# Kernel tuning notes

Measured on AMD Instinct MI355X. Metric: run time of the kernel, lower is better.

The kernel has to match this reference:

```python
import jax, jax.numpy as jnp
import numpy as np
from jax import lax

C = 128; NH = 8; DH = 16      # attn_channels, heads, head_dim
DI = 256; DS = 16; DC = 4     # hmb d_inner=expand*C, d_state, d_conv
KTOP = 128                    # max(min_focus_tokens, int(W*0.5))
CR = 64; CI = 128             # radar / image channels


def _ln(x, g, b, eps=1e-5):
    m = jnp.mean(x, -1, keepdims=True)
    v = jnp.mean((x - m) ** 2, -1, keepdims=True)
    return (x - m) * lax.rsqrt(v + eps) * g + b


def _conv1x1(x, w):
    return jnp.einsum('bchw,oc->bohw', x, w)


def _forward(image_features, radar_features, W_img, W_rad, g_q, b_q, g_kv, b_kv, g2, b2,
             Ws1, bs1, Ws2, bs2, Wqkv, bqkv, Wo, bo, Wf1, bf1, Wf2, bf2, W_delta,
             gamma, gamma_hmb, Wg, bg, Wfuse, bn_g, bn_b, bn_m, bn_v,
             W_hin, conv_dw, b_dw, W_dt, b_dt, W_Bp, W_Cp, A_log, Dp, W_hout):
    B, Cr, H, W = radar_features.shape
    N = B * H
    img_attn = _conv1x1(image_features, W_img)          # [B,C,H,W]
    rad_attn = _conv1x1(radar_features, W_rad)
    img_seq = img_attn.transpose(0, 2, 3, 1).reshape(N, W, C)
    rad_seq = rad_attn.transpose(0, 2, 3, 1).reshape(N, W, C)
    # progressive focus: per-row top-K image tokens
    si = jnp.concatenate([lax.stop_gradient(rad_seq), img_seq], -1)
    h1 = jax.nn.relu(si @ Ws1.T + bs1)
    score = (h1 @ Ws2.T + bs2)[..., 0]                  # [N,W]
    _, idx = lax.top_k(score, KTOP)
    img_kv = jnp.take_along_axis(img_seq, idx[:, :, None], axis=1)  # [N,K,C]
    # cross attention (torch MultiheadAttention, batch_first)
    q = _ln(rad_seq, g_q, b_q)
    kv = _ln(img_kv, g_kv, b_kv)
    Wq, Wk, Wv = Wqkv[:C], Wqkv[C:2 * C], Wqkv[2 * C:]
    bq_, bk_, bv_ = bqkv[:C], bqkv[C:2 * C], bqkv[2 * C:]
    qh = (q @ Wq.T + bq_).reshape(N, W, NH, DH)
    kh = (kv @ Wk.T + bk_).reshape(N, KTOP, NH, DH)
    vh = (kv @ Wv.T + bv_).reshape(N, KTOP, NH, DH)
    att = jax.nn.softmax(jnp.einsum('nqhd,nkhd->nhqk', qh, kh) / (DH ** 0.5), -1)
    ao = jnp.einsum('nhqk,nkhd->nqhd', att, vh).reshape(N, W, C) @ Wo.T + bo
    rad_seq = rad_seq + ao
    rad_seq = rad_seq + (jax.nn.relu(_ln(rad_seq, g2, b2) @ Wf1.T + bf1) @ Wf2.T + bf2)
    rad_bev = rad_seq.reshape(B, H, W, C).transpose(0, 3, 1, 2)
    delta_attn = _conv1x1(rad_bev, W_delta)
    # HMB-lite: bidirectional selective scan along x (per row)
    xz = _conv1x1(jnp.concatenate([rad_bev, img_attn], 1), W_hin)  # [B,2*DI,H,W]
    x, z = xz[:, :DI], xz[:, DI:]
    xr = x.transpose(0, 2, 1, 3).reshape(N, DI, W)
    zr = z.transpose(0, 2, 3, 1).reshape(N, W, DI)
    xp = jnp.pad(xr, ((0, 0), (0, 0), (DC - 1, 0)))     # causal depthwise conv
    xc = lax.conv_general_dilated(xp, conv_dw[:, None, :], (1,), 'VALID',
                                  feature_group_count=DI,
                                  dimension_numbers=('NCH', 'OIH', 'NCH'))
    xs = jax.nn.silu(xc + b_dw[:, None]).transpose(0, 2, 1)        # [N,W,DI]
    dt = jax.nn.softplus(xs @ W_dt.T + b_dt)            # [N,W,DI]
    Bt = xs @ W_Bp.T                                    # [N,W,DS]
    Ct = xs @ W_Cp.T
    A = -jnp.exp(A_log)                                 # [DI,DS]

    def scan(reverse):
        def step(h, inp):
            x_t, dt_t, B_t, C_t = inp
            h = jnp.exp(dt_t[..., None] * A) * h + (dt_t * x_t)[..., None] * B_t[:, None, :]
            return h, jnp.sum(h * C_t[:, None, :], -1)
        h0 = jnp.zeros((N, DI, DS), xs.dtype)
        seq = (xs.transpose(1, 0, 2), dt.transpose(1, 0, 2),
               Bt.transpose(1, 0, 2), Ct.transpose(1, 0, 2))
        _, ys = lax.scan(step, h0, seq, reverse=reverse)
        return ys.transpose(1, 0, 2)

    y = scan(False) + scan(True) + Dp * xs
    y = y * jax.nn.silu(zr)
    hmb = (y @ W_hout.T).reshape(B, H, W, C).transpose(0, 3, 1, 2)
    delta_hmb = _conv1x1(hmb, W_delta)
    # gate + range mask
    gate = jax.nn.sigmoid(_conv1x1(jnp.concatenate([radar_features, image_features], 1), Wg)
                          + bg[None, :, None, None])
    yv = jnp.arange(H, dtype=radar_features.dtype)
    wmask = jnp.clip(1.0 - 0.7 * yv / (H - 1), 0.3, None)
    gate = gate * wmask[None, None, :, None]
    radar_enh = radar_features + gamma * gate * delta_attn + gamma_hmb * gate * delta_hmb
    fuse_in = jnp.concatenate([radar_enh, image_features], 1)
    fo = lax.conv_general_dilated(fuse_in, Wfuse, (1, 1), 'SAME',
                                  dimension_numbers=('NCHW', 'OIHW', 'NCHW'))
    fo = ((fo - bn_m[None, :, None, None]) * lax.rsqrt(bn_v + 1e-5)[None, :, None, None]
          * bn_g[None, :, None, None] + bn_b[None, :, None, None])
    return jax.nn.relu(fo)


def setup_inputs():
    key = jax.random.key(0)
    ks = list(jax.random.split(key, 24))
    def rn(i, shape, s=0.05):
        return jax.random.normal(ks[i], shape, dtype=jnp.float32) * s
    B, H, W = 2, 256, 256
    return dict(
        image_features=jax.random.normal(ks[0], (B, CI, H, W), jnp.float32),
        radar_features=jax.random.normal(ks[1], (B, CR, H, W), jnp.float32),
        W_img=rn(2, (C, CI)), W_rad=rn(3, (C, CR)),
        g_q=jnp.ones(C), b_q=jnp.zeros(C), g_kv=jnp.ones(C), b_kv=jnp.zeros(C),
        g2=jnp.ones(C), b2=jnp.zeros(C),
        Ws1=rn(4, (64, 2 * C)), bs1=jnp.zeros(64), Ws2=rn(5, (1, 64)), bs2=jnp.zeros(1),
        Wqkv=rn(6, (3 * C, C)), bqkv=jnp.zeros(3 * C), Wo=rn(7, (C, C)), bo=jnp.zeros(C),
        Wf1=rn(8, (4 * C, C)), bf1=jnp.zeros(4 * C), Wf2=rn(9, (C, 4 * C)), bf2=jnp.zeros(C),
        W_delta=rn(10, (CR, C)),
        gamma=jnp.array(0.1, jnp.float32), gamma_hmb=jnp.array(0.05, jnp.float32),
        Wg=rn(11, (CR, CR + CI)), bg=jnp.zeros(CR),
        Wfuse=rn(12, (CR + CI, CR + CI, 3, 3)),
        bn_g=jnp.ones(CR + CI), bn_b=jnp.zeros(CR + CI),
        bn_m=jnp.zeros(CR + CI), bn_v=jnp.ones(CR + CI),
        W_hin=rn(13, (2 * DI, 2 * C)), conv_dw=rn(14, (DI, DC)), b_dw=jnp.zeros(DI),
        W_dt=rn(15, (DI, DI)), b_dt=jnp.full((DI,), 0.5, jnp.float32),
        W_Bp=rn(16, (DS, DI)), W_Cp=rn(17, (DS, DI)),
        A_log=jnp.log(jnp.broadcast_to(jnp.arange(1, DS + 1, dtype=jnp.float32), (DI, DS))),
        Dp=jnp.full((DI,), 0.01, jnp.float32),
        W_hout=rn(18, (C, DI)),
    )


def reference(image_features, radar_features, W_img, W_rad, g_q, b_q, g_kv, b_kv, g2, b2,
              Ws1, bs1, Ws2, bs2, Wqkv, bqkv, Wo, bo, Wf1, bf1, Wf2, bf2, W_delta,
              gamma, gamma_hmb, Wg, bg, Wfuse, bn_g, bn_b, bn_m, bn_v,
              W_hin, conv_dw, b_dw, W_dt, b_dt, W_Bp, W_Cp, A_log, Dp, W_hout):
    return _forward(image_features, radar_features, W_img, W_rad, g_q, b_q, g_kv, b_kv, g2, b2,
                    Ws1, bs1, Ws2, bs2, Wqkv, bqkv, Wo, bo, Wf1, bf1, Wf2, bf2, W_delta,
                    gamma, gamma_hmb, Wg, bg, Wfuse, bn_g, bn_b, bn_m, bn_v,
                    W_hin, conv_dw, b_dw, W_dt, b_dt, W_Bp, W_Cp, A_log, Dp, W_hout)
```

## Files before the change

### kernel.cpp

```cpp
#include <hip/hip_runtime.h>
#include <hip/hip_bf16.h>
#include <cstddef>


#define PTOK   131072
#define WSEQ   256
#define HWPIX  65536

typedef unsigned short u16;
typedef unsigned int   u32;
typedef __bf16 bf16x8 __attribute__((ext_vector_type(8)));
typedef float  f32x4  __attribute__((ext_vector_type(4)));

__device__ __forceinline__ float b2f(u16 u) { return __uint_as_float((u32)u << 16); }
__device__ __forceinline__ u16   f2b(float f) {
    u32 x = __float_as_uint(f);
    return (u16)((x + 0x7fffu + ((x >> 16) & 1u)) >> 16);
}
__device__ __forceinline__ u16 f2b_fast(float f) {
    return __builtin_bit_cast(u16, (__bf16)f);
}
__device__ __forceinline__ u32 pk2(float a, float b) {
    return (u32)f2b(a) | ((u32)f2b(b) << 16);
}
__device__ __forceinline__ void unpack8(uint4 p, float* v) {
    const u32 a[4] = {p.x, p.y, p.z, p.w};
#pragma unroll
    for (int q = 0; q < 4; ++q) {
        v[2 * q]     = b2f((u16)(a[q] & 0xffffu));
        v[2 * q + 1] = b2f((u16)(a[q] >> 16));
    }
}
__device__ __forceinline__ void load32(const u16* p, float* v) {
    uint4 a = *(const uint4*)p, b = *(const uint4*)(p + 8);
    uint4 c = *(const uint4*)(p + 16), d = *(const uint4*)(p + 24);
    unpack8(a, v); unpack8(b, v + 8); unpack8(c, v + 16); unpack8(d, v + 24);
}

constexpr int AM_NCHW = 0, AM_TOK = 1, AM_LN = 2, AM_LNG = 3, AM_CAT = 4, AM_FIN = 5;
constexpr int EP_NONE = 0, EP_RELU = 1, EP_RES = 2, EP_SP = 3;

template<int AM, int EPI>
__global__ __launch_bounds__(256)
void mgemm(const void* __restrict__ Apv, const void* __restrict__ Ap2v,
           const void* __restrict__ Ap3v, const void* __restrict__ Ap4v,
           const int* __restrict__ gidx, const float* __restrict__ stats,
           const float* __restrict__ lng, const float* __restrict__ lnb,
           const float* __restrict__ dpv,
           int K, int Cin,
           const float* __restrict__ Bw, const float* __restrict__ Bw2,
           const float* __restrict__ bias,
           u16* __restrict__ Cout, int O, int Ostride)
{
    __shared__ u16 Als[128 * 72];
    __shared__ u16 Bls[128 * 72];
    const int tid = threadIdx.x;
    const int t0 = blockIdx.x * 128;
    const int o0 = blockIdx.y * 128;
    const int lane = tid & 63, wv = tid >> 6;
    const int wm = (wv & 1) * 64, wn = (wv >> 1) * 64;
    const int fc = lane & 15, quad = lane >> 4;

    f32x4 acc[4][4];
#pragma unroll
    for (int i = 0; i < 4; ++i)
#pragma unroll
        for (int j = 0; j < 4; ++j) acc[i][j] = {0.f, 0.f, 0.f, 0.f};

    const int srow = tid >> 1;
    const int sseg = (tid & 1) * 32;

    float mrow = 0.f, rrow = 1.f;
    int grow = t0 + srow;
    if (AM == AM_LN) { mrow = stats[2 * (t0 + srow)]; rrow = stats[2 * (t0 + srow) + 1]; }
    if (AM == AM_LNG) {
        const int ar = t0 + srow;
        grow = (ar >> 7) * 256 + (gidx[ar] & 255);
        mrow = stats[2 * ar]; rrow = stats[2 * ar + 1];
    }

    for (int kc0 = 0; kc0 < K; kc0 += 64) {
        if (AM == AM_NCHW) {
            const float* Af = (const float*)Apv;
            const int tl = tid & 127, cg = (tid >> 7) * 32;
            const int t = t0 + tl;
            const size_t base = (size_t)(t >> 16) * (size_t)Cin * HWPIX + (size_t)(t & (HWPIX - 1));
#pragma unroll 8
            for (int p = 0; p < 32; ++p) {
                const int c = kc0 + cg + p;
                Als[tl * 72 + cg + p] = f2b(Af[base + (size_t)c * HWPIX]);
            }
        } else if (AM == AM_FIN) {
            const int cb = kc0 + sseg;
            const size_t base = (size_t)(t0 + srow) * 256 + cb;
            float vy[32], vb[32], vx[32], vz[32];
            load32((const u16*)Apv  + base, vy);
            load32((const u16*)Ap2v + base, vb);
            load32((const u16*)Ap3v + base, vx);
            load32((const u16*)Ap4v + base, vz);
            float v[32];
#pragma unroll
            for (int p = 0; p < 32; ++p) {
                const float dp = dpv[cb + p];
                const float zz = vz[p];
                const float tot = vy[p] + vb[p] + dp * vx[p];
                v[p] = tot * (zz / (1.f + __expf(-zz)));
            }
            uint4 q0, q1, q2, q3;
            q0.x = pk2(v[0], v[1]);   q0.y = pk2(v[2], v[3]);   q0.z = pk2(v[4], v[5]);   q0.w = pk2(v[6], v[7]);
            q1.x = pk2(v[8], v[9]);   q1.y = pk2(v[10], v[11]); q1.z = pk2(v[12], v[13]); q1.w = pk2(v[14], v[15]);
            q2.x = pk2(v[16], v[17]); q2.y = pk2(v[18], v[19]); q2.z = pk2(v[20], v[21]); q2.w = pk2(v[22], v[23]);
            q3.x = pk2(v[24], v[25]); q3.y = pk2(v[26], v[27]); q3.z = pk2(v[28], v[29]); q3.w = pk2(v[30], v[31]);
            uint4* dst = (uint4*)&Als[srow * 72 + sseg];
            dst[0] = q0; dst[1] = q1; dst[2] = q2; dst[3] = q3;
        } else {
            const u16* src; int rs, cb, row;
            if (AM == AM_CAT) {
                src = (kc0 & 128) ? (const u16*)Ap2v : (const u16*)Apv;
                rs = 128; cb = (kc0 & 127) + sseg; row = t0 + srow;
            } else if (AM == AM_LNG) {
                src = (const u16*)Apv; rs = 128; cb = kc0 + sseg; row = grow;
            } else {
                src = (const u16*)Apv; rs = K; cb = kc0 + sseg; row = t0 + srow;
            }
            const u16* rp = src + (size_t)row * rs + cb;
            uint4 pa = *(const uint4*)rp;
            uint4 pb = *(const uint4*)(rp + 8);
            uint4 pc = *(const uint4*)(rp + 16);
            uint4 pd = *(const uint4*)(rp + 24);
            if (AM == AM_LN || AM == AM_LNG) {
                float v[32];
                unpack8(pa, v); unpack8(pb, v + 8); unpack8(pc, v + 16); unpack8(pd, v + 24);
                const int c0 = cb;
#pragma unroll
                for (int p = 0; p < 32; ++p)
                    v[p] = (v[p] - mrow) * rrow * lng[c0 + p] + lnb[c0 + p];
                uint4 q0, q1, q2, q3;
                q0.x = pk2(v[0], v[1]);   q0.y = pk2(v[2], v[3]);   q0.z = pk2(v[4], v[5]);   q0.w = pk2(v[6], v[7]);
                q1.x = pk2(v[8], v[9]);   q1.y = pk2(v[10], v[11]); q1.z = pk2(v[12], v[13]); q1.w = pk2(v[14], v[15]);
                q2.x = pk2(v[16], v[17]); q2.y = pk2(v[18], v[19]); q2.z = pk2(v[20], v[21]); q2.w = pk2(v[22], v[23]);
                q3.x = pk2(v[24], v[25]); q3.y = pk2(v[26], v[27]); q3.z = pk2(v[28], v[29]); q3.w = pk2(v[30], v[31]);
                pa = q0; pb = q1; pc = q2; pd = q3;
            }
            uint4* dst = (uint4*)&Als[srow * 72 + sseg];
            dst[0] = pa; dst[1] = pb; dst[2] = pc; dst[3] = pd;
        }
        {
            const int og = o0 + srow;
            const bool ok = og < O;
            uint4 q0 = {0,0,0,0}, q1 = {0,0,0,0}, q2 = {0,0,0,0}, q3 = {0,0,0,0};
            if (ok) {
                const float* rp;
                if (Bw2 && og >= 16) rp = Bw2 + (size_t)(og - 16) * K + kc0 + sseg;
                else                 rp = Bw  + (size_t)og * K + kc0 + sseg;
                float v[32];
#pragma unroll
                for (int p = 0; p < 8; ++p) {
                    const float4 f = *(const float4*)(rp + p * 4);
                    v[p * 4 + 0] = f.x; v[p * 4 + 1] = f.y; v[p * 4 + 2] = f.z; v[p * 4 + 3] = f.w;
                }
                q0.x = pk2(v[0], v[1]);   q0.y = pk2(v[2], v[3]);   q0.z = pk2(v[4], v[5]);   q0.w = pk2(v[6], v[7]);
                q1.x = pk2(v[8], v[9]);   q1.y = pk2(v[10], v[11]); q1.z = pk2(v[12], v[13]); q1.w = pk2(v[14], v[15]);
                q2.x = pk2(v[16], v[17]); q2.y = pk2(v[18], v[19]); q2.z = pk2(v[20], v[21]); q2.w = pk2(v[22], v[23]);
                q3.x = pk2(v[24], v[25]); q3.y = pk2(v[26], v[27]); q3.z = pk2(v[28], v[29]); q3.w = pk2(v[30], v[31]);
            }
            uint4* dst = (uint4*)&Bls[srow * 72 + sseg];
            dst[0] = q0; dst[1] = q1; dst[2] = q2; dst[3] = q3;
        }
        __syncthreads();
#pragma unroll
        for (int kc = 0; kc < 64; kc += 32) {
            bf16x8 aF[4], bF[4];
#pragma unroll
            for (int mt = 0; mt < 4; ++mt)
                aF[mt] = *(const bf16x8*)&Als[(wm + mt * 16 + fc) * 72 + kc + quad * 8];
#pragma unroll
            for (int nt = 0; nt < 4; ++nt)
                bF[nt] = *(const bf16x8*)&Bls[(wn + nt * 16 + fc) * 72 + kc + quad * 8];
#pragma unroll
            for (int mt = 0; mt < 4; ++mt)
#pragma unroll
                for (int nt = 0; nt < 4; ++nt)
                    acc[mt][nt] = __builtin_amdgcn_mfma_f32_16x16x32_bf16(aF[mt], bF[nt], acc[mt][nt], 0, 0, 0);
        }
        __syncthreads();
    }

#pragma unroll
    for (int nt = 0; nt < 4; ++nt) {
        const int o = o0 + wn + nt * 16 + fc;
        if (o >= O) continue;
        const float bv = bias ? bias[o] : 0.f;
#pragma unroll
        for (int mt = 0; mt < 4; ++mt) {
#pragma unroll
            for (int reg = 0; reg < 4; ++reg) {
                const int t = t0 + wm + mt * 16 + quad * 4 + reg;
                float v = acc[mt][nt][reg] + bv;
                if (EPI == EP_RELU) v = fmaxf(v, 0.f);
                if (EPI == EP_SP)   v = fmaxf(v, 0.f) + log1pf(expf(-fabsf(v)));
                u16* dst = Cout + (size_t)t * Ostride + o;
                if (EPI == EP_RES)  v += b2f(*dst);
                *dst = f2b(v);
            }
        }
    }
}

__global__ __launch_bounds__(256)
void conv3x3_mfma(const u16* __restrict__ fin, const u16* __restrict__ Wc,
                  const float* __restrict__ bn_g, const float* __restrict__ bn_b,
                  const float* __restrict__ bn_m, const float* __restrict__ bn_v,
                  float* __restrict__ out)
{
    __shared__ u16 Als[130 * 72];
    __shared__ u16 Bls[192 * 72];
    const int tid = threadIdx.x;
    const int bid = ((int)blockIdx.x & 7) * 128 + ((int)blockIdx.x >> 3);
    const int t0 = bid * 128;
    const int lane = tid & 63, wv = tid >> 6;
    const int wm = (wv & 1) * 64, wn = (wv >> 1) * 96;
    const int fc = lane & 15, quad = lane >> 4;
    const int b = t0 >> 16, h = (t0 >> 8) & 255, w0 = t0 & 255;

    f32x4 acc[4][6];
#pragma unroll
    for (int i = 0; i < 4; ++i)
#pragma unroll
        for (int j = 0; j < 6; ++j) acc[i][j] = {0.f, 0.f, 0.f, 0.f};

    for (int kh = 0; kh < 3; ++kh) {
        const int hh = h + kh - 1;
        const bool okh = (unsigned)hh < 256u;
        const size_t rowbase = (size_t)((b * 256 + hh) * 256) * 192;
        for (int cc = 0; cc < 3; ++cc) {
            const int c0 = cc * 64;
            __syncthreads();
#pragma unroll
            for (int it = 0; it < 2; ++it) {
                const int task = tid + it * 256;
                if (task < 260) {
                    const int r = task >> 1, seg = (task & 1) * 32;
                    const int w = w0 + r - 1;
                    uint4 p0 = {0,0,0,0}, p1 = {0,0,0,0}, p2 = {0,0,0,0}, p3 = {0,0,0,0};
                    if (okh && (unsigned)w < 256u) {
                        const u16* rp = fin + rowbase + (size_t)w * 192 + c0 + seg;
                        p0 = *(const uint4*)rp;        p1 = *(const uint4*)(rp + 8);
                        p2 = *(const uint4*)(rp + 16); p3 = *(const uint4*)(rp + 24);
                    }
                    uint4* dst = (uint4*)&Als[r * 72 + seg];
                    dst[0] = p0; dst[1] = p1; dst[2] = p2; dst[3] = p3;
                }
            }
            for (int kw = 0; kw < 3; ++kw) {
                if (kw) __syncthreads();
                {
                    const int kk = kh * 3 + kw;
                    const int r0 = tid >> 1, s0 = (tid & 1) * 32;
                    const u16* rp = Wc + (size_t)kk * 36864 + (size_t)r0 * 192 + c0 + s0;
                    uint4* dst = (uint4*)&Bls[r0 * 72 + s0];
                    dst[0] = *(const uint4*)rp;        dst[1] = *(const uint4*)(rp + 8);
                    dst[2] = *(const uint4*)(rp + 16); dst[3] = *(const uint4*)(rp + 24);
                    if (tid < 128) {
                        const int r1 = 128 + r0, s1 = s0;
                        const u16* rq = Wc + (size_t)kk * 36864 + (size_t)r1 * 192 + c0 + s1;
                        uint4* dst2 = (uint4*)&Bls[r1 * 72 + s1];
                        dst2[0] = *(const uint4*)rq;        dst2[1] = *(const uint4*)(rq + 8);
                        dst2[2] = *(const uint4*)(rq + 16); dst2[3] = *(const uint4*)(rq + 24);
                    }
                }
                __syncthreads();
#pragma unroll
                for (int kc = 0; kc < 64; kc += 32) {
                    bf16x8 aF[4], bF[6];
#pragma unroll
                    for (int mt = 0; mt < 4; ++mt)
                        aF[mt] = *(const bf16x8*)&Als[(kw + wm + mt * 16 + fc) * 72 + kc + quad * 8];
#pragma unroll
                    for (int nt = 0; nt < 6; ++nt)
                        bF[nt] = *(const bf16x8*)&Bls[(wn + nt * 16 + fc) * 72 + kc + quad * 8];
#pragma unroll
                    for (int mt = 0; mt < 4; ++mt)
#pragma unroll
                        for (int nt = 0; nt < 6; ++nt)
                            acc[mt][nt] = __builtin_amdgcn_mfma_f32_16x16x32_bf16(aF[mt], bF[nt], acc[mt][nt], 0, 0, 0);
                }
            }
        }
    }

#pragma unroll
    for (int nt = 0; nt < 6; ++nt) {
        const int o = wn + nt * 16 + fc;
        const float sc = bn_g[o] * rsqrtf(bn_v[o] + 1e-5f);
        const float sh = bn_b[o] - bn_m[o] * sc;
        float* op = out + (size_t)(b * 192 + o) * HWPIX + (size_t)h * 256;
#pragma unroll
        for (int mt = 0; mt < 4; ++mt) {
#pragma unroll
            for (int reg = 0; reg < 4; ++reg) {
                const int wq = w0 + wm + mt * 16 + quad * 4 + reg;
                op[wq] = fmaxf(acc[mt][nt][reg] * sc + sh, 0.f);
            }
        }
    }
}

__global__ __launch_bounds__(256)
void stats_kernel(const u16* __restrict__ X, float* __restrict__ MR, int ntok)
{
    const int r = blockIdx.x * 4 + (threadIdx.x >> 6);
    const int lane = threadIdx.x & 63;
    if (r >= ntok) return;
    const u16* row = X + (size_t)r * 128;
    const float x0 = b2f(row[lane]), x1 = b2f(row[lane + 64]);
    float s = x0 + x1;
#pragma unroll
    for (int off = 32; off; off >>= 1) s += __shfl_xor(s, off);
    const float m = s * (1.f / 128.f);
    const float e0 = x0 - m, e1 = x1 - m;
    float v = e0 * e0 + e1 * e1;
#pragma unroll
    for (int off = 32; off; off >>= 1) v += __shfl_xor(v, off);
    if (lane == 0) { MR[2 * r] = m; MR[2 * r + 1] = rsqrtf(v * (1.f / 128.f) + 1e-5f); }
}

__global__ __launch_bounds__(256)
void kv_stats_kernel(const u16* __restrict__ I, const int* __restrict__ idx,
                     float* __restrict__ MRKV)
{
    const int r = blockIdx.x * 4 + (threadIdx.x >> 6);
    const int lane = threadIdx.x & 63;
    if (r >= 65536) return;
    const int n = r >> 7;
    const int w = idx[r] & 255;
    const u16* row = I + (size_t)(n * 256 + w) * 128;
    const float x0 = b2f(row[lane]), x1 = b2f(row[lane + 64]);
    float s = x0 + x1;
#pragma unroll
    for (int off = 32; off; off >>= 1) s += __shfl_xor(s, off);
    const float m = s * (1.f / 128.f);
    const float e0 = x0 - m, e1 = x1 - m;
    float v = e0 * e0 + e1 * e1;
#pragma unroll
    for (int off = 32; off; off >>= 1) v += __shfl_xor(v, off);
    if (lane == 0) { MRKV[2 * r] = m; MRKV[2 * r + 1] = rsqrtf(v * (1.f / 128.f) + 1e-5f); }
}

__global__ __launch_bounds__(256)
void score_select_kernel(const u16* __restrict__ radS, const u16* __restrict__ imgS,
                         const float* __restrict__ Ws1, const float* __restrict__ bs1,
                         const float* __restrict__ Ws2, const float* __restrict__ bs2,
                         int* __restrict__ idx)
{
    __shared__ float WT[256][64];
    const int tid = threadIdx.x, n = blockIdx.x;
    for (int i = tid; i < 16384; i += 256) { const int j = i >> 8, c = i & 255; WT[c][j] = Ws1[i]; }
    __syncthreads();
    float acc[64];
#pragma unroll
    for (int j = 0; j < 64; ++j) acc[j] = 0.f;
    const int t = n * WSEQ + tid;
    const u16* r0 = radS + (size_t)t * 128;
    const u16* r1 = imgS + (size_t)t * 128;
    for (int c = 0; c < 128; ++c) {
        const float v = b2f(r0[c]);
#pragma unroll
        for (int j = 0; j < 64; ++j) acc[j] += v * WT[c][j];
    }
    for (int c = 0; c < 128; ++c) {
        const float v = b2f(r1[c]);
#pragma unroll
        for (int j = 0; j < 64; ++j) acc[j] += v * WT[128 + c][j];
    }
    float s = bs2[0];
#pragma unroll
    for (int j = 0; j < 64; ++j) s += fmaxf(acc[j] + bs1[j], 0.f) * Ws2[j];
    __syncthreads();
    float* sc = &WT[0][0];
    sc[tid] = s;
    __syncthreads();
    int rank = 0;
    for (int j = 0; j < 256; ++j) {
        const float sj = sc[j];
        rank += (sj > s) || (sj == s && j < tid);
    }
    if (rank < 128) idx[n * 128 + rank] = tid;
}

__global__ __launch_bounds__(128, 2)
void attn_mfma_kernel(u16* __restrict__ qh, const u16* __restrict__ khvh)
{
    __shared__ u16 Pls[128 * 136];
    __shared__ u16 Vt[16 * 136];
    const int tid  = threadIdx.x;
    const int n    = blockIdx.x >> 1;
    const int half = blockIdx.x & 1;
    const int h    = blockIdx.y;
    const int lane = tid & 63, wv = tid >> 6;
    const int fc = lane & 15, quad = lane >> 4;
    const int wq0 = half * 128 + wv * 64;
    const int pq0 = wv * 64;

    const size_t qrow0 = (size_t)(n * 256 + wq0) * 128 + h * 16;
    const size_t krow0 = (size_t)(n * 128) * 256 + h * 16;

    {
        const int k = tid;
        const u16* src = khvh + krow0 + (size_t)k * 256 + 128;
        const uint4 a = *(const uint4*)src;
        const uint4 b = *(const uint4*)(src + 8);
        const u32 wA[4] = {a.x, a.y, a.z, a.w};
        const u32 wB[4] = {b.x, b.y, b.z, b.w};
#pragma unroll
        for (int p = 0; p < 4; ++p) {
            Vt[(2 * p)     * 136 + k] = (u16)(wA[p] & 0xffffu);
            Vt[(2 * p + 1) * 136 + k] = (u16)(wA[p] >> 16);
            Vt[(8 + 2 * p)     * 136 + k] = (u16)(wB[p] & 0xffffu);
            Vt[(8 + 2 * p + 1) * 136 + k] = (u16)(wB[p] >> 16);
        }
    }

    const uint4 z4 = {0u, 0u, 0u, 0u};
    uint4 qf[4], kf[8];
#pragma unroll
    for (int mt = 0; mt < 4; ++mt)
        qf[mt] = (quad < 2)
            ? *(const uint4*)(qh + qrow0 + (size_t)(mt * 16 + fc) * 128 + quad * 8)
            : z4;
#pragma unroll
    for (int nt = 0; nt < 8; ++nt)
        kf[nt] = (quad < 2)
            ? *(const uint4*)(khvh + krow0 + (size_t)(nt * 16 + fc) * 256 + quad * 8)
            : z4;

    f32x4 s[4][8];
#pragma unroll
    for (int mt = 0; mt < 4; ++mt)
#pragma unroll
        for (int nt = 0; nt < 8; ++nt) s[mt][nt] = {0.f, 0.f, 0.f, 0.f};
#pragma unroll
    for (int mt = 0; mt < 4; ++mt)
#pragma unroll
        for (int nt = 0; nt < 8; ++nt)
            s[mt][nt] = __builtin_amdgcn_mfma_f32_16x16x32_bf16(
                __builtin_bit_cast(bf16x8, qf[mt]),
                __builtin_bit_cast(bf16x8, kf[nt]), s[mt][nt], 0, 0, 0);

    const float cl2 = 0.25f * 1.44269504088896f;
#pragma unroll
    for (int mt = 0; mt < 4; ++mt) {
#pragma unroll
        for (int reg = 0; reg < 4; ++reg) {
            float m = s[mt][0][reg];
#pragma unroll
            for (int nt = 1; nt < 8; ++nt) m = fmaxf(m, s[mt][nt][reg]);
#pragma unroll
            for (int off = 1; off < 16; off <<= 1) m = fmaxf(m, __shfl_xor(m, off));
            const float nmc = -m * cl2;
            float l = 0.f;
#pragma unroll
            for (int nt = 0; nt < 8; ++nt) {
                const float p = exp2f(fmaf(s[mt][nt][reg], cl2, nmc));
                s[mt][nt][reg] = p;
                l += p;
            }
#pragma unroll
            for (int off = 1; off < 16; off <<= 1) l += __shfl_xor(l, off);
            const float iv = 1.f / l;
            const int prow = (pq0 + mt * 16 + quad * 4 + reg) * 136;
#pragma unroll
            for (int nt = 0; nt < 8; ++nt)
                Pls[prow + nt * 16 + fc] = f2b_fast(s[mt][nt][reg] * iv);
        }
    }

    __syncthreads();

    f32x4 o[4];
#pragma unroll
    for (int mt = 0; mt < 4; ++mt) o[mt] = {0.f, 0.f, 0.f, 0.f};
#pragma unroll
    for (int ks = 0; ks < 4; ++ks) {
        const bf16x8 vb = *(const bf16x8*)&Vt[fc * 136 + ks * 32 + quad * 8];
#pragma unroll
        for (int mt = 0; mt < 4; ++mt) {
            const bf16x8 pa = *(const bf16x8*)&Pls[(pq0 + mt * 16 + fc) * 136 + ks * 32 + quad * 8];
            o[mt] = __builtin_amdgcn_mfma_f32_16x16x32_bf16(pa, vb, o[mt], 0, 0, 0);
        }
    }

#pragma unroll
    for (int mt = 0; mt < 4; ++mt) {
#pragma unroll
        for (int reg = 0; reg < 4; ++reg) {
            qh[qrow0 + (size_t)(mt * 16 + quad * 4 + reg) * 128 + fc] = f2b_fast(o[mt][reg]);
        }
    }
}

__global__ __launch_bounds__(256)
void dwconv_kernel(u16* __restrict__ x, const float* __restrict__ kw,
                   const float* __restrict__ bdw)
{
    const int di = threadIdx.x;
    const int n = blockIdx.x;
    const float k0 = kw[di * 4 + 0], k1 = kw[di * 4 + 1];
    const float k2 = kw[di * 4 + 2], k3 = kw[di * 4 + 3];
    const float bb = bdw[di];
    float x3 = 0.f, x2 = 0.f, x1 = 0.f;
    for (int w = 0; w < 256; ++w) {
        const size_t o = (size_t)(n * WSEQ + w) * 256 + di;
        const float x0 = b2f(x[o]);
        const float v = x3 * k0 + x2 * k1 + x1 * k2 + x0 * k3 + bb;
        x[o] = f2b(v * (1.f / (1.f + __expf(-v))));
        x3 = x2; x2 = x1; x1 = x0;
    }
}

__global__ __launch_bounds__(256)
void scan_kernel(const u16* __restrict__ xs, const u16* __restrict__ dt,
                 const u16* __restrict__ btct, const float* __restrict__ A_log,
                 u16* __restrict__ yf, u16* __restrict__ yb)
{
    __shared__ float Bs[256][16];
    __shared__ float Cs[256][16];
    const int di = threadIdx.x;
    const int n = blockIdx.x & 255;
    const int dir = blockIdx.x >> 8;
    for (int i = di; i < 256 * 32; i += 256) {
        const int w = i >> 5, c = i & 31;
        const float v = b2f(btct[(size_t)(n * WSEQ + w) * 32 + c]);
        if (c < 16) Bs[w][c] = v; else Cs[w][c - 16] = v;
    }
    __syncthreads();
    float a[16];
#pragma unroll
    for (int s = 0; s < 16; ++s) a[s] = -__expf(A_log[di * 16 + s]);
    float h[16];
#pragma unroll
    for (int s = 0; s < 16; ++s) h[s] = 0.f;
    u16* yo = dir ? yb : yf;
    for (int i = 0; i < 256; ++i) {
        const int w = dir ? 255 - i : i;
        const size_t t = (size_t)(n * WSEQ + w);
        const float dtv = b2f(dt[t * 256 + di]);
        const float xv = b2f(xs[t * 256 + di]);
        const float dx = dtv * xv;
        float yv = 0.f;
#pragma unroll
        for (int s = 0; s < 16; ++s) {
            const float e = __expf(dtv * a[s]);
            h[s] = e * h[s] + dx * Bs[w][s];
            yv += h[s] * Cs[w][s];
        }
        yo[t * 256 + di] = f2b(yv);
    }
}

__global__ __launch_bounds__(256)
void precomb_kernel(const u16* __restrict__ rad3, u16* __restrict__ hmb,
                    const float* __restrict__ gamma, const float* __restrict__ gammah)
{
    const size_t i = (size_t)blockIdx.x * 256 + threadIdx.x;
    hmb[i] = f2b(gamma[0] * b2f(rad3[i]) + gammah[0] * b2f(hmb[i]));
}

__global__ __launch_bounds__(256)
void gate_kernel(const float* __restrict__ radar, const float* __restrict__ image,
                 const float* __restrict__ Wg, const float* __restrict__ bg,
                 const u16* __restrict__ dcomb, u16* __restrict__ fin)
{
    __shared__ float WT[192][64];
    const int tid = threadIdx.x;
    const int bh = blockIdx.x;
    const int b = bh >> 8, h = bh & 255;
    for (int i = tid; i < 64 * 192; i += 256) { const int o = i / 192, c = i % 192; WT[c][o] = Wg[i]; }
    __syncthreads();
    float acc[64];
#pragma unroll
    for (int o = 0; o < 64; ++o) acc[o] = 0.f;
    const size_t rbase = (size_t)b * 64 * HWPIX + (size_t)h * 256 + tid;
    const size_t ibase = (size_t)b * 128 * HWPIX + (size_t)h * 256 + tid;
    for (int c = 0; c < 64; ++c) {
        const float v = radar[rbase + (size_t)c * HWPIX];
#pragma unroll
        for (int o = 0; o < 64; ++o) acc[o] += v * WT[c][o];
    }
    for (int c = 0; c < 128; ++c) {
        const float v = image[ibase + (size_t)c * HWPIX];
#pragma unroll
        for (int o = 0; o < 64; ++o) acc[o] += v * WT[64 + c][o];
    }
    const float wm = fmaxf(1.f - 0.7f * (float)h * (1.f / 255.f), 0.3f);
    const size_t t = (size_t)bh * 256 + tid;
    u16* fo = fin + t * 192;
    for (int o = 0; o < 64; ++o) {
        const float gate = wm / (1.f + __expf(-(acc[o] + bg[o])));
        fo[o] = f2b(radar[rbase + (size_t)o * HWPIX] + gate * b2f(dcomb[t * 64 + o]));
    }
    for (int c = 0; c < 128; ++c)
        fo[64 + c] = f2b(image[ibase + (size_t)c * HWPIX]);
}

__global__ __launch_bounds__(256)
void wprep_kernel(const float* __restrict__ Wfuse, u16* __restrict__ Wc)
{
    const int i = blockIdx.x * 256 + threadIdx.x;
    if (i >= 9 * 192 * 192) return;
    const int kk = i / 36864, r = i % 36864;
    const int o = r / 192, c = r % 192;
    Wc[i] = f2b(Wfuse[o * 1728 + c * 9 + kk]);
}

extern "C" void kernel_launch(void* const* d_in, const int* in_sizes, int n_in,
                              void* d_out, int out_size, void* d_ws, size_t ws_size,
                              hipStream_t stream)
{
    const float* image  = (const float*)d_in[0];
    const float* radar  = (const float*)d_in[1];
    const float* W_img  = (const float*)d_in[2];
    const float* W_rad  = (const float*)d_in[3];
    const float* g_q    = (const float*)d_in[4];
    const float* b_q    = (const float*)d_in[5];
    const float* g_kv   = (const float*)d_in[6];
    const float* b_kv   = (const float*)d_in[7];
    const float* g2     = (const float*)d_in[8];
    const float* b2     = (const float*)d_in[9];
    const float* Ws1    = (const float*)d_in[10];
    const float* bs1    = (const float*)d_in[11];
    const float* Ws2    = (const float*)d_in[12];
    const float* bs2    = (const float*)d_in[13];
    const float* Wqkv   = (const float*)d_in[14];
    const float* bqkv   = (const float*)d_in[15];
    const float* Wo     = (const float*)d_in[16];
    const float* bo     = (const float*)d_in[17];
    const float* Wf1    = (const float*)d_in[18];
    const float* bf1    = (const float*)d_in[19];
    const float* Wf2    = (const float*)d_in[20];
    const float* bf2    = (const float*)d_in[21];
    const float* W_delta= (const float*)d_in[22];
    const float* gamma  = (const float*)d_in[23];
    const float* gammah = (const float*)d_in[24];
    const float* Wg     = (const float*)d_in[25];
    const float* bg     = (const float*)d_in[26];
    const float* Wfuse  = (const float*)d_in[27];
    const float* bn_g   = (const float*)d_in[28];
    const float* bn_b   = (const float*)d_in[29];
    const float* bn_m   = (const float*)d_in[30];
    const float* bn_v   = (const float*)d_in[31];
    const float* W_hin  = (const float*)d_in[32];
    const float* conv_dw= (const float*)d_in[33];
    const float* b_dw   = (const float*)d_in[34];
    const float* W_dt   = (const float*)d_in[35];
    const float* b_dt   = (const float*)d_in[36];
    const float* W_Bp   = (const float*)d_in[37];
    const float* W_Cp   = (const float*)d_in[38];
    const float* A_log  = (const float*)d_in[39];
    const float* Dp     = (const float*)d_in[40];
    const float* W_hout = (const float*)d_in[41];
    float* out = (float*)d_out;

    u16* wsu = (u16*)d_ws;
    u16* R = wsu;
    u16* I = wsu + 16777216u;
    u16* U = wsu + 33554432u;
    u16* V = wsu + 67108864u;
    u16* Wc = wsu + 100663296u;
    float* ftail = (float*)(wsu + 100995072u);
    float* MR    = ftail;
    float* MRKV  = ftail + 262144u;
    int*   IDX   = (int*)(ftail + 393216u);

    u16* ob  = (u16*)d_out;
    u16* QH  = ob;
    u16* KVH = ob + 16777216u;
    u16* T1  = ob;
    u16* DT  = ob;
    u16* BC  = ob + 16777216u;
    u16* YF  = ob + 18874368u;
    u16* HMB = ob + 35651584u;
    u16* YB  = I;
    u16* DC  = V;

    wprep_kernel<<<1296, 256, 0, stream>>>(Wfuse, Wc);

    mgemm<AM_NCHW, EP_NONE><<<dim3(1024, 1), 256, 0, stream>>>(image, nullptr, nullptr, nullptr, nullptr, nullptr, nullptr, nullptr, nullptr, 128, 128, W_img, nullptr, nullptr, I, 128, 128);
    mgemm<AM_NCHW, EP_NONE><<<dim3(1024, 1), 256, 0, stream>>>(radar, nullptr, nullptr, nullptr, nullptr, nullptr, nullptr, nullptr, nullptr,  64,  64, W_rad, nullptr, nullptr, R, 128, 128);

    score_select_kernel<<<512, 256, 0, stream>>>(R, I, Ws1, bs1, Ws2, bs2, IDX);

    stats_kernel<<<32768, 256, 0, stream>>>(R, MR, PTOK);
    kv_stats_kernel<<<16384, 256, 0, stream>>>(I, IDX, MRKV);

    mgemm<AM_LN,  EP_NONE><<<dim3(1024, 1), 256, 0, stream>>>(R, nullptr, nullptr, nullptr, nullptr, MR, g_q, b_q, nullptr, 128, 0, Wqkv, nullptr, bqkv, QH, 128, 128);
    mgemm<AM_LNG, EP_NONE><<<dim3(512, 2), 256, 0, stream>>>(I, nullptr, nullptr, nullptr, IDX, MRKV, g_kv, b_kv, nullptr, 128, 0, Wqkv + 16384, nullptr, bqkv + 128, KVH, 256, 256);

    attn_mfma_kernel<<<dim3(1024, 8), 128, 0, stream>>>(QH, KVH);
    mgemm<AM_TOK, EP_RES><<<dim3(1024, 1), 256, 0, stream>>>(QH, nullptr, nullptr, nullptr, nullptr, nullptr, nullptr, nullptr, nullptr, 128, 0, Wo, nullptr, bo, R, 128, 128);

    stats_kernel<<<32768, 256, 0, stream>>>(R, MR, PTOK);
    for (int hfl = 0; hfl < 2; ++hfl) {
        const size_t off = (size_t)hfl * 65536u;
        mgemm<AM_LN,  EP_RELU><<<dim3(512, 4), 256, 0, stream>>>(R + off * 128, nullptr, nullptr, nullptr, nullptr, MR + off * 2, g2, b2, nullptr, 128, 0, Wf1, nullptr, bf1, T1, 512, 512);
        mgemm<AM_TOK, EP_RES ><<<dim3(512, 1), 256, 0, stream>>>(T1, nullptr, nullptr, nullptr, nullptr, nullptr, nullptr, nullptr, nullptr, 512, 0, Wf2, nullptr, bf2, R + off * 128, 128, 128);
    }

    mgemm<AM_CAT, EP_NONE><<<dim3(1024, 2), 256, 0, stream>>>(R, I, nullptr, nullptr, nullptr, nullptr, nullptr, nullptr, nullptr, 256, 0, W_hin, nullptr, nullptr, U, 256, 256);
    mgemm<AM_CAT, EP_NONE><<<dim3(1024, 2), 256, 0, stream>>>(R, I, nullptr, nullptr, nullptr, nullptr, nullptr, nullptr, nullptr, 256, 0, W_hin + 65536, nullptr, nullptr, V, 256, 256);

    dwconv_kernel<<<512, 256, 0, stream>>>(U, conv_dw, b_dw);

    for (int hfl = 0; hfl < 2; ++hfl) {
        const size_t off = (size_t)hfl * 65536u;
        u16* xs = U + off * 256;
        u16* z  = V + off * 256;
        mgemm<AM_TOK, EP_SP  ><<<dim3(512, 2), 256, 0, stream>>>(xs, nullptr, nullptr, nullptr, nullptr, nullptr, nullptr, nullptr, nullptr, 256, 0, W_dt, nullptr, b_dt, DT, 256, 256);
        mgemm<AM_TOK, EP_NONE><<<dim3(512, 1), 256, 0, stream>>>(xs, nullptr, nullptr, nullptr, nullptr, nullptr, nullptr, nullptr, nullptr, 256, 0, W_Bp, W_Cp, nullptr, BC, 32, 32);
        scan_kernel<<<512, 256, 0, stream>>>(xs, DT, BC, A_log, YF, YB);
        mgemm<AM_FIN, EP_NONE><<<dim3(512, 1), 256, 0, stream>>>(YF, YB, xs, z, nullptr, nullptr, nullptr, nullptr, Dp, 256, 0, W_hout, nullptr, nullptr, HMB, 128, 128);
        precomb_kernel<<<32768, 256, 0, stream>>>(R + off * 128, HMB, gamma, gammah);
        mgemm<AM_TOK, EP_NONE><<<dim3(512, 1), 256, 0, stream>>>(HMB, nullptr, nullptr, nullptr, nullptr, nullptr, nullptr, nullptr, nullptr, 128, 0, W_delta, nullptr, nullptr, DC + off * 64, 64, 64);
    }

    gate_kernel<<<512, 256, 0, stream>>>(radar, image, Wg, bg, DC, U);

    conv3x3_mfma<<<dim3(1024), 256, 0, stream>>>(U, Wc, bn_g, bn_b, bn_m, bn_v, out);
}
```

Measured before the change: 1.963 ms.

## Load conv3x3 weights directly from fragment-ordered global layout, skip LDS staging

The weight-prep kernel now writes the 3x3 fusion weights in MFMA B-fragment order, so each lane of the conv3x3 kernel loads its bf16x8 weight fragments straight from global memory. This removes the shared-memory B tile and the two barriers per kw step. The warp tiling changes from 2x2 (64 rows x 96 cols) to 1x4 (128 rows x 48 cols), and the epilogue writes float4 vectors. The cost is that weights are re-read from global/L2 by every block with no LDS reuse, and more A fragments are read from LDS per wave.

```diff
diff --git a/kernel.cpp b/kernel.cpp
--- a/kernel.cpp
+++ b/kernel.cpp
@@ -214,20 +214,19 @@
                   float* __restrict__ out)
 {
     __shared__ u16 Als[130 * 72];
-    __shared__ u16 Bls[192 * 72];
     const int tid = threadIdx.x;
     const int bid = ((int)blockIdx.x & 7) * 128 + ((int)blockIdx.x >> 3);
     const int t0 = bid * 128;
     const int lane = tid & 63, wv = tid >> 6;
-    const int wm = (wv & 1) * 64, wn = (wv >> 1) * 96;
+    const int wn = wv * 48;
     const int fc = lane & 15, quad = lane >> 4;
     const int b = t0 >> 16, h = (t0 >> 8) & 255, w0 = t0 & 255;
 
-    f32x4 acc[4][6];
-#pragma unroll
-    for (int i = 0; i < 4; ++i)
-#pragma unroll
-        for (int j = 0; j < 6; ++j) acc[i][j] = {0.f, 0.f, 0.f, 0.f};
+    f32x4 acc[8][3];
+#pragma unroll
+    for (int i = 0; i < 8; ++i)
+#pragma unroll
+        for (int j = 0; j < 3; ++j) acc[i][j] = {0.f, 0.f, 0.f, 0.f};
 
     for (int kh = 0; kh < 3; ++kh) {
         const int hh = h + kh - 1;
@@ -252,56 +251,44 @@
                     dst[0] = p0; dst[1] = p1; dst[2] = p2; dst[3] = p3;
                 }
             }
+            __syncthreads();
+#pragma unroll
             for (int kw = 0; kw < 3; ++kw) {
-                if (kw) __syncthreads();
-                {
-                    const int kk = kh * 3 + kw;
-                    const int r0 = tid >> 1, s0 = (tid & 1) * 32;
-                    const u16* rp = Wc + (size_t)kk * 36864 + (size_t)r0 * 192 + c0 + s0;
-                    uint4* dst = (uint4*)&Bls[r0 * 72 + s0];
-                    dst[0] = *(const uint4*)rp;        dst[1] = *(const uint4*)(rp + 8);
-                    dst[2] = *(const uint4*)(rp + 16); dst[3] = *(const uint4*)(rp + 24);
-                    if (tid < 128) {
-                        const int r1 = 128 + r0, s1 = s0;
-                        const u16* rq = Wc + (size_t)kk * 36864 + (size_t)r1 * 192 + c0 + s1;
-                        uint4* dst2 = (uint4*)&Bls[r1 * 72 + s1];
-                        dst2[0] = *(const uint4*)rq;        dst2[1] = *(const uint4*)(rq + 8);
-                        dst2[2] = *(const uint4*)(rq + 16); dst2[3] = *(const uint4*)(rq + 24);
+                const int kk = kh * 3 + kw;
+                const u16* wb = Wc + (size_t)(kk * 3 + cc) * 12288;
+#pragma unroll
+                for (int khalf = 0; khalf < 2; ++khalf) {
+                    bf16x8 bF[3];
+#pragma unroll
+                    for (int nt = 0; nt < 3; ++nt)
+                        bF[nt] = *(const bf16x8*)&wb[(size_t)((khalf * 12 + wv * 3 + nt) * 64 + lane) * 8];
+                    const int kc = khalf * 32;
+#pragma unroll
+                    for (int mt = 0; mt < 8; ++mt) {
+                        const bf16x8 aF = *(const bf16x8*)&Als[(kw + mt * 16 + fc) * 72 + kc + quad * 8];
+#pragma unroll
+                        for (int nt = 0; nt < 3; ++nt)
+                            acc[mt][nt] = __builtin_amdgcn_mfma_f32_16x16x32_bf16(aF, bF[nt], acc[mt][nt], 0, 0, 0);
                     }
                 }
-                __syncthreads();
-#pragma unroll
-                for (int kc = 0; kc < 64; kc += 32) {
-                    bf16x8 aF[4], bF[6];
-#pragma unroll
-                    for (int mt = 0; mt < 4; ++mt)
-                        aF[mt] = *(const bf16x8*)&Als[(kw + wm + mt * 16 + fc) * 72 + kc + quad * 8];
-#pragma unroll
-                    for (int nt = 0; nt < 6; ++nt)
-                        bF[nt] = *(const bf16x8*)&Bls[(wn + nt * 16 + fc) * 72 + kc + quad * 8];
-#pragma unroll
-                    for (int mt = 0; mt < 4; ++mt)
-#pragma unroll
-                        for (int nt = 0; nt < 6; ++nt)
-                            acc[mt][nt] = __builtin_amdgcn_mfma_f32_16x16x32_bf16(aF[mt], bF[nt], acc[mt][nt], 0, 0, 0);
-                }
-            }
-        }
-    }
-
-#pragma unroll
-    for (int nt = 0; nt < 6; ++nt) {
+            }
+        }
+    }
+
+#pragma unroll
+    for (int nt = 0; nt < 3; ++nt) {
         const int o = wn + nt * 16 + fc;
         const float sc = bn_g[o] * rsqrtf(bn_v[o] + 1e-5f);
         const float sh = bn_b[o] - bn_m[o] * sc;
         float* op = out + (size_t)(b * 192 + o) * HWPIX + (size_t)h * 256;
 #pragma unroll
-        for (int mt = 0; mt < 4; ++mt) {
-#pragma unroll
-            for (int reg = 0; reg < 4; ++reg) {
-                const int wq = w0 + wm + mt * 16 + quad * 4 + reg;
-                op[wq] = fmaxf(acc[mt][nt][reg] * sc + sh, 0.f);
-            }
+        for (int mt = 0; mt < 8; ++mt) {
+            float4 vv;
+            vv.x = fmaxf(acc[mt][nt][0] * sc + sh, 0.f);
+            vv.y = fmaxf(acc[mt][nt][1] * sc + sh, 0.f);
+            vv.z = fmaxf(acc[mt][nt][2] * sc + sh, 0.f);
+            vv.w = fmaxf(acc[mt][nt][3] * sc + sh, 0.f);
+            *(float4*)(op + w0 + mt * 16 + quad * 4) = vv;
         }
     }
 }
@@ -610,7 +597,13 @@
     if (i >= 9 * 192 * 192) return;
     const int kk = i / 36864, r = i % 36864;
     const int o = r / 192, c = r % 192;
-    Wc[i] = f2b(Wfuse[o * 1728 + c * 9 + kk]);
+    const int cc = c >> 6, c64 = c & 63;
+    const int kh2 = c64 >> 5, c32 = c64 & 31;
+    const int quad = c32 >> 3, e = c32 & 7;
+    const int ot = o >> 4, fc = o & 15;
+    const size_t dst = ((size_t)(((kk * 3 + cc) * 2 + kh2) * 12 + ot) * 64
+                        + quad * 16 + fc) * 8 + e;
+    Wc[dst] = f2b(Wfuse[o * 1728 + c * 9 + kk]);
 }
 
 extern "C" void kernel_launch(void* const* d_in, const int* in_sizes, int n_in,
```

Result: faster. 1.850 ms (-5.7%).
